# Kernel optimization log

Hardware: AMD Instinct MI355X
Metric: run time of the kernel (lower is better)

Reference implementation:

```python
import jax
import jax.numpy as jnp
from jax import lax
import numpy as np


def design_butter_hp_sos(order: int, cutoff: float, fs: float) -> np.ndarray:
    """Pure-numpy replica of scipy.signal.butter(order, cutoff, 'hp', fs=fs, output='sos')."""
    Wn = cutoff / (fs / 2.0)          # normalized to Nyquist
    fs_b = 2.0                        # scipy's internal sampling rate convention
    warped = 2.0 * fs_b * np.tan(np.pi * Wn / fs_b)  # prewarped analog cutoff
    # Analog Butterworth lowpass prototype poles (buttap)
    m = np.arange(-order + 1, order, 2)
    p_lp = -np.exp(1j * np.pi * m / (2 * order))
    k = np.real(np.prod(-p_lp))       # == 1 for Butterworth
    # lp2hp: zeros at s=0, poles -> warped / p
    p_hp = warped / p_lp
    z_hp = np.zeros(order, dtype=complex)
    # bilinear transform (fs2 = 2 * fs_b)
    fs2 = 2.0 * fs_b
    p_z = (fs2 + p_hp) / (fs2 - p_hp)
    k_z = k * np.real(np.prod(fs2 - z_hp) / np.prod(fs2 - p_hp))
    # pair conjugate poles into biquads; scipy puts poles nearest unit circle LAST
    pos = p_z[np.imag(p_z) > 0]
    pos = pos[np.argsort(np.abs(pos))]
    n_sec = order // 2
    sos = np.zeros((n_sec, 6))
    for i, p in enumerate(pos):
        b = np.array([1.0, -2.0, 1.0])  # two zeros at z = 1 (DC block)
        if i == 0:
            b = b * k_z                 # overall gain lives in the first section
        sos[i, :3] = b
        sos[i, 3:] = np.array([1.0, -2.0 * p.real, np.abs(p) ** 2])
    return sos.astype(np.float32)


def setup_inputs() -> dict:
    key = jax.random.key(0)
    audio = jax.random.normal(key, (64, 480000), dtype=jnp.float32)  # [batch, samples]
    sos = jnp.asarray(design_butter_hp_sos(4, 80.0, 16000.0))        # [2, 6]
    return {"audio": audio, "sos": sos}


def _sosfilt(sos, x):
    """Cascade biquad IIR (direct form II transposed), zero initial state.
    x: [B, T], sos: [n_sections, 6]. Batch is vectorized inside the scan carry."""
    B = x.shape[0]

    def one_section(x, coefs):
        b0, b1, b2, _, a1, a2 = coefs

        def step(state, xn):
            s0, s1 = state                 # each [B]
            y = b0 * xn + s0
            s0_new = b1 * xn - a1 * y + s1
            s1_new = b2 * xn - a2 * y
            return (s0_new, s1_new), y

        init = (jnp.zeros(B, x.dtype), jnp.zeros(B, x.dtype))
        _, y = lax.scan(step, init, x.T)   # scan over time, [T, B]
        return y.T

    for i in range(sos.shape[0]):          # small static loop over 2 sections
        x = one_section(x, sos[i])
    return x


def reference(audio, sos):
    squeeze = audio.ndim == 1
    x = audio[None, :] if squeeze else audio
    y = _sosfilt(sos, x)
    return y[0] if squeeze else y
```

## Files before the change

kernel.cpp:

```cpp
#include <hip/hip_runtime.h>


#define SEG   32
#define F4S   8
#define NT    32
#define SEGS  256
#define EMITS (SEGS - NT)
#define NWAVE 4

typedef float f32x4 __attribute__((ext_vector_type(4)));

struct Coefs { float b00,b01,b02,a01,a02,b10,b11,b12,a11,a12; };

__device__ __forceinline__ void step(const Coefs& c, float xn,
    float& s10, float& s11, float& s20, float& s21, float& yout) {
  float y1 = fmaf(c.b00, xn, s10);
  s10 = fmaf(-c.a01, y1, fmaf(c.b01, xn, s11));
  s11 = fmaf(-c.a02, y1, c.b02 * xn);
  float y2 = fmaf(c.b10, y1, s20);
  s20 = fmaf(-c.a11, y2, fmaf(c.b11, y1, s21));
  s21 = fmaf(-c.a12, y2, c.b12 * y1);
  yout = y2;
}

__device__ __forceinline__ Coefs load_coefs(const float* __restrict__ sos) {
  Coefs c;
  c.b00=sos[0]; c.b01=sos[1]; c.b02=sos[2]; c.a01=sos[4];  c.a02=sos[5];
  c.b10=sos[6]; c.b11=sos[7]; c.b12=sos[8]; c.a11=sos[10]; c.a12=sos[11];
  return c;
}

__device__ __forceinline__ f32x4 matvec(const float* __restrict__ m, f32x4 v) {
  f32x4 r;
  r[0] = fmaf(m[0],  v[0], fmaf(m[1],  v[1], fmaf(m[2],  v[2], m[3]  * v[3])));
  r[1] = fmaf(m[4],  v[0], fmaf(m[5],  v[1], fmaf(m[6],  v[2], m[7]  * v[3])));
  r[2] = fmaf(m[8],  v[0], fmaf(m[9],  v[1], fmaf(m[10], v[2], m[11] * v[3])));
  r[3] = fmaf(m[12], v[0], fmaf(m[13], v[1], fmaf(m[14], v[2], m[15] * v[3])));
  return r;
}

__global__ void iir_setup(const float* __restrict__ sos, float* __restrict__ ws) {
  if (blockIdx.x != 0 || threadIdx.x != 0) return;
  Coefs c = load_coefs(sos);
  float P[16];
  {
    float A[16];
    for (int col = 0; col < 4; ++col) {
      float a0 = (col == 0), a1 = (col == 1), a2 = (col == 2), a3 = (col == 3), dd;
      step(c, 0.f, a0, a1, a2, a3, dd);
      A[0*4+col] = a0; A[1*4+col] = a1; A[2*4+col] = a2; A[3*4+col] = a3;
    }
    for (int i = 0; i < 16; ++i) P[i] = A[i];
    for (int it = 0; it < 5; ++it) {
      float Q[16];
      for (int r = 0; r < 4; ++r)
        for (int cc = 0; cc < 4; ++cc) {
          float acc = 0.f;
          for (int kk = 0; kk < 4; ++kk) acc = fmaf(P[r*4+kk], P[kk*4+cc], acc);
          Q[r*4+cc] = acc;
        }
      for (int i = 0; i < 16; ++i) P[i] = Q[i];
    }
  }
  for (int l = 0; l < 7; ++l) {
    for (int i = 0; i < 16; ++i) ws[l*16 + i] = P[i];
    float Q[16];
    for (int r = 0; r < 4; ++r)
      for (int cc = 0; cc < 4; ++cc) {
        float acc = 0.f;
        for (int kk = 0; kk < 4; ++kk) acc = fmaf(P[r*4+kk], P[kk*4+cc], acc);
        Q[r*4+cc] = acc;
      }
    for (int i = 0; i < 16; ++i) P[i] = Q[i];
  }
}

__global__ __launch_bounds__(256, 4) void iir_fused(
    const float* __restrict__ x, const float* __restrict__ sos,
    const float* __restrict__ ws, float* __restrict__ out,
    int T, int nchunks, int bpr) {
  __shared__ f32x4 stg[SEGS * F4S];
  __shared__ f32x4 wtot[NWAVE];

  int row = blockIdx.x / bpr;
  int blk = blockIdx.x - row * bpr;
  int k = threadIdx.x;
  int lane = k & 63, wid = k >> 6;
  int sbase = blk * EMITS - NT;
  int myseg = sbase + k;
  int perm = k & 7;
  Coefs c = load_coefs(sos);

  const f32x4* xr4 = reinterpret_cast<const f32x4*>(x) + (size_t)row * (T >> 2);
  f32x4*       yr4 = reinterpret_cast<f32x4*>(out)     + (size_t)row * (T >> 2);
  const f32x4 z4 = {0.f, 0.f, 0.f, 0.f};

  f32x4 t0,t1,t2,t3,t4,t5,t6,t7;
#define PREF(IT, TR) { int f_ = k + IT*256; int s_ = f_>>3; int gs_ = sbase + s_; \
    TR = (gs_ >= 0 && gs_ < nchunks) ? xr4[(size_t)gs_ * F4S + (f_&7)] : z4; }
#define WST(IT, TR) { int f_ = k + IT*256; int s_ = f_>>3, j_ = f_&7; \
    stg[s_*F4S + (j_^(s_&7))] = TR; }
  PREF(0,t0) PREF(1,t1) PREF(2,t2) PREF(3,t3)
  PREF(4,t4) PREF(5,t5) PREF(6,t6) PREF(7,t7)
  WST(0,t0) WST(1,t1) WST(2,t2) WST(3,t3)
  WST(4,t4) WST(5,t5) WST(6,t6) WST(7,t7)
  __syncthreads();

  f32x4 u;
  {
    float s10 = 0.f, s11 = 0.f, s20 = 0.f, s21 = 0.f, d_;
#pragma unroll
    for (int j = 0; j < F4S; ++j) {
      f32x4 v = stg[k * F4S + (j ^ perm)];
      step(c, v[0], s10, s11, s20, s21, d_);
      step(c, v[1], s10, s11, s20, s21, d_);
      step(c, v[2], s10, s11, s20, s21, d_);
      step(c, v[3], s10, s11, s20, s21, d_);
    }
    u[0] = s10; u[1] = s11; u[2] = s20; u[3] = s21;
  }

  f32x4 I = u;
#pragma unroll
  for (int l = 0; l < 6; ++l) {
    int off = 1 << l;
    f32x4 w;
    w[0] = __shfl_up(I[0], off, 64);
    w[1] = __shfl_up(I[1], off, 64);
    w[2] = __shfl_up(I[2], off, 64);
    w[3] = __shfl_up(I[3], off, 64);
    if (lane >= off) {
      f32x4 pv = matvec(ws + l * 16, w);
      I[0] += pv[0]; I[1] += pv[1]; I[2] += pv[2]; I[3] += pv[3];
    }
  }
  if (lane == 63) wtot[wid] = I;
  __syncthreads();

  f32x4 carry = z4;
  if (wid > 0) {
    carry = wtot[0];
    const float* p64 = ws + 6 * 16;
#pragma unroll
    for (int p = 1; p < NWAVE - 1; ++p)
      if (p <= wid - 1) {
        f32x4 pc = matvec(p64, carry);
        carry[0] = wtot[p][0] + pc[0]; carry[1] = wtot[p][1] + pc[1];
        carry[2] = wtot[p][2] + pc[2]; carry[3] = wtot[p][3] + pc[3];
      }
  }

  if (lane == 0) {
    f32x4 pc = matvec(ws, carry);
    u[0] += pc[0]; u[1] += pc[1]; u[2] += pc[2]; u[3] += pc[3];
  }
  I = u;
#pragma unroll
  for (int l = 0; l < 6; ++l) {
    int off = 1 << l;
    f32x4 w;
    w[0] = __shfl_up(I[0], off, 64);
    w[1] = __shfl_up(I[1], off, 64);
    w[2] = __shfl_up(I[2], off, 64);
    w[3] = __shfl_up(I[3], off, 64);
    if (lane >= off) {
      f32x4 pv = matvec(ws + l * 16, w);
      I[0] += pv[0]; I[1] += pv[1]; I[2] += pv[2]; I[3] += pv[3];
    }
  }
  f32x4 S;
  S[0] = __shfl_up(I[0], 1, 64);
  S[1] = __shfl_up(I[1], 1, 64);
  S[2] = __shfl_up(I[2], 1, 64);
  S[3] = __shfl_up(I[3], 1, 64);
  if (lane == 0) S = carry;

  bool emits = (k >= NT) && (myseg < nchunks);
  if (emits) {
    float s10 = S[0], s11 = S[1], s20 = S[2], s21 = S[3];
#pragma unroll
    for (int j = 0; j < F4S; ++j) {
      f32x4 v = stg[k * F4S + (j ^ perm)];
      f32x4 yv; float yo;
      step(c, v[0], s10, s11, s20, s21, yo); yv[0] = yo;
      step(c, v[1], s10, s11, s20, s21, yo); yv[1] = yo;
      step(c, v[2], s10, s11, s20, s21, yo); yv[2] = yo;
      step(c, v[3], s10, s11, s20, s21, yo); yv[3] = yo;
      stg[k * F4S + (j ^ perm)] = yv;
    }
  }
  __syncthreads();

  int eseg0 = blk * EMITS;
  int nemit = nchunks - eseg0; if (nemit > EMITS) nemit = EMITS;
  if (nemit > 0) {
    int F = nemit * F4S;
    f32x4* dst = yr4 + (size_t)eseg0 * F4S;
    for (int f = k; f < F; f += 256) {
      int s = f >> 3, j = f & 7;
      int ls = s + NT;
      dst[f] = stg[ls * F4S + (j ^ (ls & 7))];
    }
  }
}

#define FB_C 256
#define FB_W 1024
__global__ __launch_bounds__(256) void sosfilt2_chunked(
    const float* __restrict__ x, const float* __restrict__ sos,
    float* __restrict__ out, int B, int T, int nchunks) {
  int tid = blockIdx.x * 256 + threadIdx.x;
  if (tid >= B * nchunks) return;
  int row = tid / nchunks;
  int chunk = tid - row * nchunks;
  Coefs c = load_coefs(sos);
  const float* xr = x + (size_t)row * T;
  float*       yr = out + (size_t)row * T;
  int c0   = chunk * FB_C;
  int cend = min(c0 + FB_C, T);
  int warm = min(FB_W, c0);
  int t    = c0 - warm;
  float s10 = 0.f, s11 = 0.f, s20 = 0.f, s21 = 0.f;
  float dump;
  for (; t < c0; t += 4) {
    f32x4 xvv = *reinterpret_cast<const f32x4*>(xr + t);
#pragma unroll
    for (int j = 0; j < 4; ++j) step(c, xvv[j], s10, s11, s20, s21, dump);
  }
  int tv_end = c0 + ((cend - c0) & ~3);
  for (; t < tv_end; t += 4) {
    f32x4 xvv = *reinterpret_cast<const f32x4*>(xr + t);
    f32x4 yv;
#pragma unroll
    for (int j = 0; j < 4; ++j) {
      float yo;
      step(c, xvv[j], s10, s11, s20, s21, yo);
      yv[j] = yo;
    }
    *reinterpret_cast<f32x4*>(yr + t) = yv;
  }
  for (; t < cend; ++t) { float yv; step(c, xr[t], s10, s11, s20, s21, yv); yr[t] = yv; }
}

extern "C" void kernel_launch(void* const* d_in, const int* in_sizes, int n_in,
                              void* d_out, int out_size, void* d_ws, size_t ws_size,
                              hipStream_t stream) {
  const float* x   = (const float*)d_in[0];
  const float* sos = (const float*)d_in[1];
  float*       out = (float*)d_out;

  int total = in_sizes[0];
  int T = 480000;
  if (total % T != 0) T = total;
  int B = total / T;

  if (T % SEG == 0 && ws_size >= 112 * sizeof(float)) {
    float* ws = (float*)d_ws;
    int nchunks = T / SEG;
    int bpr = (nchunks + EMITS - 1) / EMITS;
    iir_setup<<<1, 64, 0, stream>>>(sos, ws);
    iir_fused<<<B * bpr, 256, 0, stream>>>(x, sos, ws, out, T, nchunks, bpr);
  } else {
    int nc = (T + FB_C - 1) / FB_C;
    int grid = (B * nc + 255) / 256;
    sosfilt2_chunked<<<grid, 256, 0, stream>>>(x, sos, out, B, T, nc);
  }
}
```

Measured before the change: 54.54 us.

## Halve segment length, widen warm-up, and double-buffer two tiles per block

Each thread now handles 16-sample segments instead of 32, and the warm-up region grows to 64 segments so that the same 1024-sample warm-up depth is kept. Each block processes two consecutive tiles and prefetches the next tile's input into registers while the current tile is scanned, using two shared-memory buffers with a rotated slot layout. The aim is shorter serial recurrence chains per thread and global-load latency hidden behind compute. The cost is that only 192 of 256 segments per tile emit output, a larger redundant fraction than before, plus a longer-running block.

```diff
diff --git a/kernel.cpp b/kernel.cpp
--- a/kernel.cpp
+++ b/kernel.cpp
@@ -1,12 +1,13 @@
 #include <hip/hip_runtime.h>
 
 
-#define SEG   32
-#define F4S   8
-#define NT    32
+#define SEG   16
+#define F4S   4
+#define NT    64
 #define SEGS  256
 #define EMITS (SEGS - NT)
 #define NWAVE 4
+#define TPB   2
 
 typedef float f32x4 __attribute__((ext_vector_type(4)));
 
@@ -51,7 +52,7 @@
       A[0*4+col] = a0; A[1*4+col] = a1; A[2*4+col] = a2; A[3*4+col] = a3;
     }
     for (int i = 0; i < 16; ++i) P[i] = A[i];
-    for (int it = 0; it < 5; ++it) {
+    for (int it = 0; it < 4; ++it) {
       float Q[16];
       for (int r = 0; r < 4; ++r)
         for (int cc = 0; cc < 4; ++cc) {
@@ -75,131 +76,150 @@
   }
 }
 
+#define SLOT(S, J) (((J) + ((S) >> 1)) & 3)
+
 __global__ __launch_bounds__(256, 4) void iir_fused(
     const float* __restrict__ x, const float* __restrict__ sos,
     const float* __restrict__ ws, float* __restrict__ out,
-    int T, int nchunks, int bpr) {
-  __shared__ f32x4 stg[SEGS * F4S];
+    int T, int nchunks, int bpr, int tiles_row) {
+  __shared__ f32x4 stg[2][SEGS * F4S];
   __shared__ f32x4 wtot[NWAVE];
 
   int row = blockIdx.x / bpr;
   int blk = blockIdx.x - row * bpr;
   int k = threadIdx.x;
   int lane = k & 63, wid = k >> 6;
-  int sbase = blk * EMITS - NT;
-  int myseg = sbase + k;
-  int perm = k & 7;
   Coefs c = load_coefs(sos);
 
   const f32x4* xr4 = reinterpret_cast<const f32x4*>(x) + (size_t)row * (T >> 2);
   f32x4*       yr4 = reinterpret_cast<f32x4*>(out)     + (size_t)row * (T >> 2);
   const f32x4 z4 = {0.f, 0.f, 0.f, 0.f};
 
-  f32x4 t0,t1,t2,t3,t4,t5,t6,t7;
-#define PREF(IT, TR) { int f_ = k + IT*256; int s_ = f_>>3; int gs_ = sbase + s_; \
-    TR = (gs_ >= 0 && gs_ < nchunks) ? xr4[(size_t)gs_ * F4S + (f_&7)] : z4; }
-#define WST(IT, TR) { int f_ = k + IT*256; int s_ = f_>>3, j_ = f_&7; \
-    stg[s_*F4S + (j_^(s_&7))] = TR; }
-  PREF(0,t0) PREF(1,t1) PREF(2,t2) PREF(3,t3)
-  PREF(4,t4) PREF(5,t5) PREF(6,t6) PREF(7,t7)
-  WST(0,t0) WST(1,t1) WST(2,t2) WST(3,t3)
-  WST(4,t4) WST(5,t5) WST(6,t6) WST(7,t7)
-  __syncthreads();
-
-  f32x4 u;
-  {
-    float s10 = 0.f, s11 = 0.f, s20 = 0.f, s21 = 0.f, d_;
-#pragma unroll
-    for (int j = 0; j < F4S; ++j) {
-      f32x4 v = stg[k * F4S + (j ^ perm)];
-      step(c, v[0], s10, s11, s20, s21, d_);
-      step(c, v[1], s10, s11, s20, s21, d_);
-      step(c, v[2], s10, s11, s20, s21, d_);
-      step(c, v[3], s10, s11, s20, s21, d_);
-    }
-    u[0] = s10; u[1] = s11; u[2] = s20; u[3] = s21;
-  }
-
-  f32x4 I = u;
-#pragma unroll
-  for (int l = 0; l < 6; ++l) {
-    int off = 1 << l;
-    f32x4 w;
-    w[0] = __shfl_up(I[0], off, 64);
-    w[1] = __shfl_up(I[1], off, 64);
-    w[2] = __shfl_up(I[2], off, 64);
-    w[3] = __shfl_up(I[3], off, 64);
-    if (lane >= off) {
-      f32x4 pv = matvec(ws + l * 16, w);
-      I[0] += pv[0]; I[1] += pv[1]; I[2] += pv[2]; I[3] += pv[3];
-    }
-  }
-  if (lane == 63) wtot[wid] = I;
-  __syncthreads();
-
-  f32x4 carry = z4;
-  if (wid > 0) {
-    carry = wtot[0];
-    const float* p64 = ws + 6 * 16;
-#pragma unroll
-    for (int p = 1; p < NWAVE - 1; ++p)
-      if (p <= wid - 1) {
-        f32x4 pc = matvec(p64, carry);
+  f32x4 t0, t1, t2, t3;
+#define PREF(TILE) { int sb_ = (TILE) * EMITS - NT;                         \
+    { int f_=k;       int s_=f_>>2; int gs_=sb_+s_;                         \
+      t0 = (gs_>=0 && gs_<nchunks) ? xr4[(size_t)gs_*F4S + (f_&3)] : z4; }  \
+    { int f_=k+256;   int s_=f_>>2; int gs_=sb_+s_;                         \
+      t1 = (gs_>=0 && gs_<nchunks) ? xr4[(size_t)gs_*F4S + (f_&3)] : z4; }  \
+    { int f_=k+512;   int s_=f_>>2; int gs_=sb_+s_;                         \
+      t2 = (gs_>=0 && gs_<nchunks) ? xr4[(size_t)gs_*F4S + (f_&3)] : z4; }  \
+    { int f_=k+768;   int s_=f_>>2; int gs_=sb_+s_;                         \
+      t3 = (gs_>=0 && gs_<nchunks) ? xr4[(size_t)gs_*F4S + (f_&3)] : z4; } }
+#define WST(BUF) {                                                          \
+    { int f_=k;     int s_=f_>>2, j_=f_&3; stg[BUF][s_*F4S+SLOT(s_,j_)]=t0; } \
+    { int f_=k+256; int s_=f_>>2, j_=f_&3; stg[BUF][s_*F4S+SLOT(s_,j_)]=t1; } \
+    { int f_=k+512; int s_=f_>>2, j_=f_&3; stg[BUF][s_*F4S+SLOT(s_,j_)]=t2; } \
+    { int f_=k+768; int s_=f_>>2, j_=f_&3; stg[BUF][s_*F4S+SLOT(s_,j_)]=t3; } }
+
+  int tile0 = blk * TPB;
+  if (tile0 >= tiles_row) return;
+  PREF(tile0)
+
+  for (int ti = 0; ti < TPB; ++ti) {
+    int tile = tile0 + ti;
+    if (tile >= tiles_row) break;
+    int buf = ti & 1;
+    int sbase = tile * EMITS - NT;
+    int myseg = sbase + k;
+
+    WST(buf)
+    __syncthreads();
+    if (ti + 1 < TPB && tile + 1 < tiles_row)
+      PREF(tile + 1)
+
+    f32x4 u;
+    {
+      float s10 = 0.f, s11 = 0.f, s20 = 0.f, s21 = 0.f, d_;
+#pragma unroll
+      for (int j = 0; j < F4S; ++j) {
+        f32x4 v = stg[buf][k * F4S + SLOT(k, j)];
+        step(c, v[0], s10, s11, s20, s21, d_);
+        step(c, v[1], s10, s11, s20, s21, d_);
+        step(c, v[2], s10, s11, s20, s21, d_);
+        step(c, v[3], s10, s11, s20, s21, d_);
+      }
+      u[0] = s10; u[1] = s11; u[2] = s20; u[3] = s21;
+    }
+
+    f32x4 I = u;
+#pragma unroll
+    for (int l = 0; l < 6; ++l) {
+      int off = 1 << l;
+      f32x4 w;
+      w[0] = __shfl_up(I[0], off, 64);
+      w[1] = __shfl_up(I[1], off, 64);
+      w[2] = __shfl_up(I[2], off, 64);
+      w[3] = __shfl_up(I[3], off, 64);
+      if (lane >= off) {
+        f32x4 pv = matvec(ws + l * 16, w);
+        I[0] += pv[0]; I[1] += pv[1]; I[2] += pv[2]; I[3] += pv[3];
+      }
+    }
+    if (lane == 63) wtot[wid] = I;
+    __syncthreads();
+
+    f32x4 carry = z4;
+    const float* p1024 = ws + 6 * 16;
+#pragma unroll
+    for (int p = 0; p < NWAVE - 1; ++p) {
+      if (p < wid) {
+        f32x4 pc = matvec(p1024, carry);
         carry[0] = wtot[p][0] + pc[0]; carry[1] = wtot[p][1] + pc[1];
         carry[2] = wtot[p][2] + pc[2]; carry[3] = wtot[p][3] + pc[3];
       }
-  }
-
-  if (lane == 0) {
-    f32x4 pc = matvec(ws, carry);
-    u[0] += pc[0]; u[1] += pc[1]; u[2] += pc[2]; u[3] += pc[3];
-  }
-  I = u;
-#pragma unroll
-  for (int l = 0; l < 6; ++l) {
-    int off = 1 << l;
-    f32x4 w;
-    w[0] = __shfl_up(I[0], off, 64);
-    w[1] = __shfl_up(I[1], off, 64);
-    w[2] = __shfl_up(I[2], off, 64);
-    w[3] = __shfl_up(I[3], off, 64);
-    if (lane >= off) {
-      f32x4 pv = matvec(ws + l * 16, w);
-      I[0] += pv[0]; I[1] += pv[1]; I[2] += pv[2]; I[3] += pv[3];
-    }
-  }
-  f32x4 S;
-  S[0] = __shfl_up(I[0], 1, 64);
-  S[1] = __shfl_up(I[1], 1, 64);
-  S[2] = __shfl_up(I[2], 1, 64);
-  S[3] = __shfl_up(I[3], 1, 64);
-  if (lane == 0) S = carry;
-
-  bool emits = (k >= NT) && (myseg < nchunks);
-  if (emits) {
-    float s10 = S[0], s11 = S[1], s20 = S[2], s21 = S[3];
-#pragma unroll
-    for (int j = 0; j < F4S; ++j) {
-      f32x4 v = stg[k * F4S + (j ^ perm)];
-      f32x4 yv; float yo;
-      step(c, v[0], s10, s11, s20, s21, yo); yv[0] = yo;
-      step(c, v[1], s10, s11, s20, s21, yo); yv[1] = yo;
-      step(c, v[2], s10, s11, s20, s21, yo); yv[2] = yo;
-      step(c, v[3], s10, s11, s20, s21, yo); yv[3] = yo;
-      stg[k * F4S + (j ^ perm)] = yv;
-    }
-  }
-  __syncthreads();
-
-  int eseg0 = blk * EMITS;
-  int nemit = nchunks - eseg0; if (nemit > EMITS) nemit = EMITS;
-  if (nemit > 0) {
-    int F = nemit * F4S;
-    f32x4* dst = yr4 + (size_t)eseg0 * F4S;
-    for (int f = k; f < F; f += 256) {
-      int s = f >> 3, j = f & 7;
-      int ls = s + NT;
-      dst[f] = stg[ls * F4S + (j ^ (ls & 7))];
+    }
+
+    if (lane == 0) {
+      f32x4 pc = matvec(ws, carry);
+      u[0] += pc[0]; u[1] += pc[1]; u[2] += pc[2]; u[3] += pc[3];
+    }
+    I = u;
+#pragma unroll
+    for (int l = 0; l < 6; ++l) {
+      int off = 1 << l;
+      f32x4 w;
+      w[0] = __shfl_up(I[0], off, 64);
+      w[1] = __shfl_up(I[1], off, 64);
+      w[2] = __shfl_up(I[2], off, 64);
+      w[3] = __shfl_up(I[3], off, 64);
+      if (lane >= off) {
+        f32x4 pv = matvec(ws + l * 16, w);
+        I[0] += pv[0]; I[1] += pv[1]; I[2] += pv[2]; I[3] += pv[3];
+      }
+    }
+    f32x4 S;
+    S[0] = __shfl_up(I[0], 1, 64);
+    S[1] = __shfl_up(I[1], 1, 64);
+    S[2] = __shfl_up(I[2], 1, 64);
+    S[3] = __shfl_up(I[3], 1, 64);
+    if (lane == 0) S = carry;
+
+    bool emits = (k >= NT) && (myseg < nchunks);
+    if (emits) {
+      float s10 = S[0], s11 = S[1], s20 = S[2], s21 = S[3];
+#pragma unroll
+      for (int j = 0; j < F4S; ++j) {
+        f32x4 v = stg[buf][k * F4S + SLOT(k, j)];
+        f32x4 yv; float yo;
+        step(c, v[0], s10, s11, s20, s21, yo); yv[0] = yo;
+        step(c, v[1], s10, s11, s20, s21, yo); yv[1] = yo;
+        step(c, v[2], s10, s11, s20, s21, yo); yv[2] = yo;
+        step(c, v[3], s10, s11, s20, s21, yo); yv[3] = yo;
+        stg[buf][k * F4S + SLOT(k, j)] = yv;
+      }
+    }
+    __syncthreads();
+
+    int eseg0 = tile * EMITS;
+    int nemit = nchunks - eseg0; if (nemit > EMITS) nemit = EMITS;
+    if (nemit > 0) {
+      int F = nemit * F4S;
+      f32x4* dst = yr4 + (size_t)eseg0 * F4S;
+      for (int f = k; f < F; f += 256) {
+        int s = f >> 2, j = f & 3;
+        int ls = s + NT;
+        dst[f] = stg[buf][ls * F4S + SLOT(ls, j)];
+      }
     }
   }
 }
@@ -257,9 +277,10 @@
   if (T % SEG == 0 && ws_size >= 112 * sizeof(float)) {
     float* ws = (float*)d_ws;
     int nchunks = T / SEG;
-    int bpr = (nchunks + EMITS - 1) / EMITS;
+    int tiles_row = (nchunks + EMITS - 1) / EMITS;
+    int bpr = (tiles_row + TPB - 1) / TPB;
     iir_setup<<<1, 64, 0, stream>>>(sos, ws);
-    iir_fused<<<B * bpr, 256, 0, stream>>>(x, sos, ws, out, T, nchunks, bpr);
+    iir_fused<<<B * bpr, 256, 0, stream>>>(x, sos, ws, out, T, nchunks, bpr, tiles_row);
   } else {
     int nc = (T + FB_C - 1) / FB_C;
     int grid = (B * nc + 255) / 256;
```

Result: slower. 66.77 us (+22.4%).
